# Performance work log

Measured on AMD Instinct MI355X. Metric: run time of the kernel, lower is better.

Reference implementation:

```python
import jax, jax.numpy as jnp
import numpy as np
import math

MASK_FILL = -1e6  # d2l masked_softmax fills masked scores with -1e6


def setup_inputs() -> dict:
    key = jax.random.key(0)
    kq, kk, kv, kl = jax.random.split(key, 4)
    B, Lq, Lk, D = 16, 2048, 2048, 64
    queries = jax.random.normal(kq, (B, Lq, D), dtype=jnp.float32)
    keys = jax.random.normal(kk, (B, Lk, D), dtype=jnp.float32)
    values = jax.random.normal(kv, (B, Lk, D), dtype=jnp.float32)
    valid_lens = jax.random.randint(kl, (B,), 1, Lk + 1, dtype=jnp.int32)
    return {"queries": queries, "keys": keys, "values": values, "valid_lens": valid_lens}


def reference(queries, keys, values, valid_lens):
    # scores: [B, Lq, Lk]
    d = queries.shape[-1]
    scores = jnp.einsum("bqd,bkd->bqk", queries, keys) / math.sqrt(d)
    # masked_softmax: positions >= valid_lens[b] along key axis get -1e6
    Lk = keys.shape[1]
    mask = jnp.arange(Lk)[None, None, :] < valid_lens[:, None, None]  # [B,1,Lk]
    scores = jnp.where(mask, scores, MASK_FILL)
    attn = jax.nn.softmax(scores, axis=-1)
    # dropout p=0.0 (eval) is identity
    return jnp.einsum("bqk,bkd->bqd", attn, values)
```

## Files before the change

kernel.cpp:

```cpp
#include <hip/hip_runtime.h>
#include <hip/hip_bf16.h>
#include <stdint.h>


#define BATCH 16
#define SEQ   2048
#define DIM   64
#define QBLK  32
#define NSPLIT 4
#define NTHR  256

typedef __bf16 bf16x8 __attribute__((ext_vector_type(8)));
typedef float  f32x16 __attribute__((ext_vector_type(16)));
typedef unsigned int u32x2 __attribute__((ext_vector_type(2)));

static constexpr float QSCALE = 0.125f * 1.44269504088896340736f;

__device__ __forceinline__ uint32_t pk2bf(float a, float b) {
    union { __hip_bfloat162 h; uint32_t u; } c;
    c.h = __float22bfloat162_rn(make_float2(a, b));
    return c.u;
}
__device__ __forceinline__ bf16x8 mk8(uint32_t w0, uint32_t w1, uint32_t w2, uint32_t w3) {
    union { uint32_t u[4]; bf16x8 v; } c;
    c.u[0] = w0; c.u[1] = w1; c.u[2] = w2; c.u[3] = w3;
    return c.v;
}
__device__ __forceinline__ u32x2 plswap(uint32_t a, uint32_t b) {
    return __builtin_amdgcn_permlane32_swap(a, b, false, false);
}
__device__ __forceinline__ float vmax16(const f32x16& v) {
    float a = fmaxf(fmaxf(v[0], v[1]), fmaxf(v[2], v[3]));
    float b = fmaxf(fmaxf(v[4], v[5]), fmaxf(v[6], v[7]));
    float c = fmaxf(fmaxf(v[8], v[9]), fmaxf(v[10], v[11]));
    float d = fmaxf(fmaxf(v[12], v[13]), fmaxf(v[14], v[15]));
    return fmaxf(fmaxf(a, b), fmaxf(c, d));
}
__device__ __forceinline__ float vsum16(const f32x16& v) {
    float a = (v[0] + v[1]) + (v[2] + v[3]);
    float b = (v[4] + v[5]) + (v[6] + v[7]);
    float c = (v[8] + v[9]) + (v[10] + v[11]);
    float d = (v[12] + v[13]) + (v[14] + v[15]);
    return (a + b) + (c + d);
}

__global__ __launch_bounds__(256) void prep_kv(
        const float* __restrict__ K, const float* __restrict__ V,
        unsigned short* __restrict__ Kbf, unsigned short* __restrict__ Vt)
{
    __shared__ float tl[64][65];
    const int bid = blockIdx.x;
    const int b  = bid >> 5;
    const int kb = (bid & 31) * 64;
    const int tid = threadIdx.x;

    const float* Kp = K + ((size_t)b * SEQ + kb) * DIM;
    const float* Vp = V + ((size_t)b * SEQ + kb) * DIM;
    unsigned short* Ko = Kbf + ((size_t)b * SEQ + kb) * DIM;
    unsigned short* Vo = Vt + (size_t)b * SEQ * DIM + (size_t)(kb >> 5) * 2048;

    #pragma unroll
    for (int p = 0; p < 4; ++p) {
        int idx = p * 256 + tid;
        float4 x = ((const float4*)Kp)[idx];
        ((uint2*)Ko)[idx] = make_uint2(pk2bf(x.x, x.y), pk2bf(x.z, x.w));
    }
    #pragma unroll
    for (int p = 0; p < 4; ++p) {
        int idx = p * 256 + tid;
        int r = idx >> 4, c = (idx & 15) * 4;
        float4 x = *(const float4*)(Vp + r * DIM + c);
        tl[r][c] = x.x; tl[r][c+1] = x.y; tl[r][c+2] = x.z; tl[r][c+3] = x.w;
    }
    __syncthreads();
    #pragma unroll
    for (int p = 0; p < 4; ++p) {
        int idx = p * 256 + tid;
        int sub = idx >> 9;
        int rem = idx & 511;
        int d  = rem >> 3;
        int kq = (rem & 7) * 4;
        int kr = sub * 32 + kq;
        *(uint2*)(Vo + sub * 2048 + d * 32 + kq) =
            make_uint2(pk2bf(tl[kr][d],     tl[kr + 1][d]),
                       pk2bf(tl[kr + 2][d], tl[kr + 3][d]));
    }
}

__global__ __launch_bounds__(NTHR, 2) void attn_main(
        const float* __restrict__ Q, const unsigned short* __restrict__ Kbf,
        const unsigned short* __restrict__ Vt, const int* __restrict__ VL,
        float* __restrict__ O)
{
    __shared__ float comb[NSPLIT - 1][2176];

    const int tid  = threadIdx.x;
    const int idx  = blockIdx.x;
    const int g    = idx >> 8;
    const int u    = idx & 255;
    const int b    = ((u & 15) + g) & (BATCH - 1);
    const int qt   = (u >> 4) + g * 16;
    const int qb   = qt * QBLK;
    const int split = tid >> 6;
    const int lane = tid & 63;
    const int h    = lane >> 5;
    const int ln   = lane & 31;

    const int valid  = VL[b];
    const int ntiles = (valid + 31) >> 5;

    const size_t bOff = (size_t)b * SEQ * DIM;
    const int qrow = qb + ln;

    bf16x8 qf[4];
    {
        const float* qp = Q + bOff + (size_t)qrow * DIM;
        #pragma unroll
        for (int s = 0; s < 4; ++s) {
            int c0 = s * 16 + h * 8;
            float4 x = *(const float4*)(qp + c0);
            float4 y = *(const float4*)(qp + c0 + 4);
            qf[s] = mk8(pk2bf(x.x * QSCALE, x.y * QSCALE),
                        pk2bf(x.z * QSCALE, x.w * QSCALE),
                        pk2bf(y.x * QSCALE, y.y * QSCALE),
                        pk2bf(y.z * QSCALE, y.w * QSCALE));
        }
    }

    f32x16 o0, o1;
    #pragma unroll
    for (int r = 0; r < 16; ++r) { o0[r] = 0.0f; o1[r] = 0.0f; }
    float m_run = -1e30f, l_run = 0.0f;

    const unsigned short* kp = Kbf + bOff + (size_t)ln * DIM + h * 8;
    const unsigned short* vp = Vt  + bOff + (size_t)ln * 32  + h * 8;

    bf16x8 ka[4], va[4];
    int kt = split;
    if (kt < ntiles) {
        const unsigned short* kq = kp + (size_t)kt * 2048;
        const unsigned short* vq = vp + (size_t)kt * 2048;
        #pragma unroll
        for (int s = 0; s < 4; ++s) ka[s] = *(const bf16x8*)(kq + s * 16);
        va[0] = *(const bf16x8*)(vq);
        va[1] = *(const bf16x8*)(vq + 16);
        va[2] = *(const bf16x8*)(vq + 1024);
        va[3] = *(const bf16x8*)(vq + 1024 + 16);
    }

    for (; kt < ntiles; kt += NSPLIT) {
        const int ktn = (kt + NSPLIT < ntiles) ? kt + NSPLIT : kt;
        bf16x8 kan[4], van[4];
        {
            const unsigned short* kq = kp + (size_t)ktn * 2048;
            const unsigned short* vq = vp + (size_t)ktn * 2048;
            #pragma unroll
            for (int s = 0; s < 4; ++s) kan[s] = *(const bf16x8*)(kq + s * 16);
            van[0] = *(const bf16x8*)(vq);
            van[1] = *(const bf16x8*)(vq + 16);
            van[2] = *(const bf16x8*)(vq + 1024);
            van[3] = *(const bf16x8*)(vq + 1024 + 16);
        }

        f32x16 st;
        #pragma unroll
        for (int r = 0; r < 16; ++r) st[r] = 0.0f;
        #pragma unroll
        for (int s = 0; s < 4; ++s)
            st = __builtin_amdgcn_mfma_f32_32x32x16_bf16(ka[s], qf[s], st, 0, 0, 0);

        const int kb = kt * 32;
        if (kb + 32 > valid) {
            #pragma unroll
            for (int r = 0; r < 16; ++r) {
                int krel = (r & 3) + 8 * (r >> 2) + 4 * h;
                if (kb + krel >= valid) st[r] = -1e30f;
            }
        }

        float pm = vmax16(st);
        u32x2 sm = plswap(__float_as_uint(pm), __float_as_uint(pm));
        pm = fmaxf(__uint_as_float(sm[0]), __uint_as_float(sm[1]));
        if (!__all(pm <= m_run + 8.0f)) {
            float mnew = fmaxf(m_run, pm);
            float sc = __builtin_exp2f(m_run - mnew);
            l_run *= sc;
            #pragma unroll
            for (int r = 0; r < 16; ++r) { o0[r] *= sc; o1[r] *= sc; }
            m_run = mnew;
        }
        #pragma unroll
        for (int r = 0; r < 16; ++r) st[r] = __builtin_exp2f(st[r] - m_run);
        float ps = vsum16(st);
        u32x2 ss = plswap(__float_as_uint(ps), __float_as_uint(ps));
        l_run += __uint_as_float(ss[0]) + __uint_as_float(ss[1]);

        uint32_t W00 = pk2bf(st[0],  st[1]),  W01 = pk2bf(st[2],  st[3]);
        uint32_t W10 = pk2bf(st[4],  st[5]),  W11 = pk2bf(st[6],  st[7]);
        uint32_t W20 = pk2bf(st[8],  st[9]),  W21 = pk2bf(st[10], st[11]);
        uint32_t W30 = pk2bf(st[12], st[13]), W31 = pk2bf(st[14], st[15]);
        u32x2 sA = plswap(W00, W10), sB = plswap(W01, W11);
        bf16x8 bp0 = mk8(sA[0], sB[0], sA[1], sB[1]);
        u32x2 sC = plswap(W20, W30), sD = plswap(W21, W31);
        bf16x8 bp1 = mk8(sC[0], sD[0], sC[1], sD[1]);

        o0 = __builtin_amdgcn_mfma_f32_32x32x16_bf16(va[0], bp0, o0, 0, 0, 0);
        o1 = __builtin_amdgcn_mfma_f32_32x32x16_bf16(va[2], bp0, o1, 0, 0, 0);
        o0 = __builtin_amdgcn_mfma_f32_32x32x16_bf16(va[1], bp1, o0, 0, 0, 0);
        o1 = __builtin_amdgcn_mfma_f32_32x32x16_bf16(va[3], bp1, o1, 0, 0, 0);

        #pragma unroll
        for (int i = 0; i < 4; ++i) { ka[i] = kan[i]; va[i] = van[i]; }
    }

    if (split != 0) {
        float* base = comb[split - 1];
        #pragma unroll
        for (int r = 0; r < 16; ++r) {
            base[r * 64 + lane]        = o0[r];
            base[(r + 16) * 64 + lane] = o1[r];
        }
        base[2048 + lane]      = m_run;
        base[2048 + 64 + lane] = l_run;
    }
    __syncthreads();
    if (split == 0) {
        float M = m_run;
        #pragma unroll
        for (int j = 0; j < NSPLIT - 1; ++j)
            M = fmaxf(M, comb[j][2048 + lane]);
        float sc0 = __builtin_exp2f(m_run - M);
        float lt = l_run * sc0;
        #pragma unroll
        for (int r = 0; r < 16; ++r) { o0[r] *= sc0; o1[r] *= sc0; }
        #pragma unroll
        for (int j = 0; j < NSPLIT - 1; ++j) {
            float mj = comb[j][2048 + lane];
            float lj = comb[j][2048 + 64 + lane];
            float scj = __builtin_exp2f(mj - M);
            lt += lj * scj;
            #pragma unroll
            for (int r = 0; r < 16; ++r) {
                o0[r] += scj * comb[j][r * 64 + lane];
                o1[r] += scj * comb[j][(r + 16) * 64 + lane];
            }
        }
        float inv = 1.0f / lt;
        float* op = O + bOff + (size_t)qrow * DIM;
        #pragma unroll
        for (int a = 0; a < 4; ++a) {
            float4 w0, w1;
            w0.x = o0[4*a+0] * inv; w0.y = o0[4*a+1] * inv;
            w0.z = o0[4*a+2] * inv; w0.w = o0[4*a+3] * inv;
            w1.x = o1[4*a+0] * inv; w1.y = o1[4*a+1] * inv;
            w1.z = o1[4*a+2] * inv; w1.w = o1[4*a+3] * inv;
            *(float4*)(op + 8*a + 4*h)      = w0;
            *(float4*)(op + 32 + 8*a + 4*h) = w1;
        }
    }
}

__device__ __forceinline__ uint32_t swz(uint32_t row, uint32_t colByte) {
    return row * 128u + (colByte ^ ((row & 7u) << 4));
}
__device__ __forceinline__ bf16x8 lds8(const char* p) {
    union { uint4 q; bf16x8 v; } c;
    c.q = *(const uint4*)p;
    return c.v;
}

__global__ __launch_bounds__(256, 2) void attn_fallback(
        const float* __restrict__ Q, const float* __restrict__ K,
        const float* __restrict__ V, const int* __restrict__ VL,
        float* __restrict__ O)
{
    __shared__ unsigned short lds[2][2][64 * DIM];
    const int tid  = threadIdx.x;
    const int bid  = blockIdx.x;
    const int b    = bid & (BATCH - 1);
    const int qt   = bid >> 4;
    const int qb   = qt * 64;
    const int qhalf = (tid >> 6) & 1;
    const int split = tid >> 7;
    const int lane = tid & 63;
    const int h    = lane >> 5;
    const int ln   = lane & 31;
    const int ptid = tid & 127;

    const int valid  = VL[b];
    const int ntiles = (valid + 63) / 64;
    const int nit    = (ntiles + 1) / 2;

    const size_t bOff = (size_t)b * SEQ * DIM;
    const int qrow = qb + qhalf * 32 + ln;

    bf16x8 qf[4];
    {
        const float* qp = Q + bOff + (size_t)qrow * DIM;
        #pragma unroll
        for (int s = 0; s < 4; ++s) {
            int c0 = s * 16 + h * 8;
            float4 x = *(const float4*)(qp + c0);
            float4 y = *(const float4*)(qp + c0 + 4);
            qf[s] = mk8(pk2bf(x.x * QSCALE, x.y * QSCALE),
                        pk2bf(x.z * QSCALE, x.w * QSCALE),
                        pk2bf(y.x * QSCALE, y.y * QSCALE),
                        pk2bf(y.z * QSCALE, y.w * QSCALE));
        }
    }
    f32x16 o0, o1;
    #pragma unroll
    for (int r = 0; r < 16; ++r) { o0[r] = 0.0f; o1[r] = 0.0f; }
    float m_run = -1e30f, l_run = 0.0f;
    const float* Kb = K + bOff;
    const float* Vb = V + bOff;
    char* kls = (char*)lds[split][0];
    char* vls = (char*)lds[split][1];

    for (int it = 0; it < nit; ++it) {
        const int kt = it * 2 + split;
        const bool act = kt < ntiles;
        const int kb = kt * 64;
        if (act) {
            #pragma unroll
            for (int p = 0; p < 8; ++p) {
                int idx = p * 128 + ptid;
                int r = idx >> 4, c = (idx & 15) * 4;
                float4 kx = *(const float4*)(Kb + (size_t)(kb + r) * DIM + c);
                *(uint2*)(kls + swz(r, c * 2)) =
                    make_uint2(pk2bf(kx.x, kx.y), pk2bf(kx.z, kx.w));
            }
            #pragma unroll
            for (int p = 0; p < 2; ++p) {
                int idx = p * 128 + ptid;
                int cq = idx & 15, rq = idx >> 4;
                const float* vp = Vb + (size_t)(kb + rq * 4) * DIM + cq * 4;
                float4 v0 = *(const float4*)(vp);
                float4 v1 = *(const float4*)(vp + DIM);
                float4 v2 = *(const float4*)(vp + 2 * DIM);
                float4 v3 = *(const float4*)(vp + 3 * DIM);
                float a0[4] = {v0.x, v0.y, v0.z, v0.w};
                float a1[4] = {v1.x, v1.y, v1.z, v1.w};
                float a2[4] = {v2.x, v2.y, v2.z, v2.w};
                float a3[4] = {v3.x, v3.y, v3.z, v3.w};
                #pragma unroll
                for (int i = 0; i < 4; ++i)
                    *(uint2*)(vls + swz(cq * 4 + i, rq * 8)) =
                        make_uint2(pk2bf(a0[i], a1[i]), pk2bf(a2[i], a3[i]));
            }
        }
        __syncthreads();
        if (act) {
            f32x16 st0, st1;
            #pragma unroll
            for (int r = 0; r < 16; ++r) { st0[r] = 0.0f; st1[r] = 0.0f; }
            #pragma unroll
            for (int s = 0; s < 4; ++s) {
                int cb = (s * 16 + h * 8) * 2;
                bf16x8 ka0 = lds8(kls + swz(ln,      cb));
                bf16x8 ka1 = lds8(kls + swz(ln + 32, cb));
                st0 = __builtin_amdgcn_mfma_f32_32x32x16_bf16(ka0, qf[s], st0, 0, 0, 0);
                st1 = __builtin_amdgcn_mfma_f32_32x32x16_bf16(ka1, qf[s], st1, 0, 0, 0);
            }
            if (kb + 64 > valid) {
                #pragma unroll
                for (int r = 0; r < 16; ++r) {
                    int krel = (r & 3) + 8 * (r >> 2) + 4 * h;
                    if (kb + krel      >= valid) st0[r] = -1e30f;
                    if (kb + 32 + krel >= valid) st1[r] = -1e30f;
                }
            }
            float pm = fmaxf(vmax16(st0), vmax16(st1));
            u32x2 sm = plswap(__float_as_uint(pm), __float_as_uint(pm));
            pm = fmaxf(__uint_as_float(sm[0]), __uint_as_float(sm[1]));
            float mnew = fmaxf(m_run, pm);
            float sc = __builtin_exp2f(m_run - mnew);
            #pragma unroll
            for (int r = 0; r < 16; ++r) {
                st0[r] = __builtin_exp2f(st0[r] - mnew);
                st1[r] = __builtin_exp2f(st1[r] - mnew);
            }
            float ps = vsum16(st0) + vsum16(st1);
            u32x2 ss = plswap(__float_as_uint(ps), __float_as_uint(ps));
            ps = __uint_as_float(ss[0]) + __uint_as_float(ss[1]);
            l_run = l_run * sc + ps;
            m_run = mnew;
            #pragma unroll
            for (int r = 0; r < 16; ++r) { o0[r] *= sc; o1[r] *= sc; }
            bf16x8 bp[4];
            {
                uint32_t u0 = pk2bf(st0[0], st0[1]),  u1 = pk2bf(st0[2], st0[3]);
                uint32_t u2 = pk2bf(st0[4], st0[5]),  u3 = pk2bf(st0[6], st0[7]);
                uint32_t u4 = pk2bf(st0[8], st0[9]),  u5 = pk2bf(st0[10], st0[11]);
                uint32_t u6 = pk2bf(st0[12], st0[13]), u7 = pk2bf(st0[14], st0[15]);
                u32x2 s02 = plswap(u0, u2), s13 = plswap(u1, u3);
                bp[0] = mk8(s02[0], s13[0], s02[1], s13[1]);
                u32x2 s46 = plswap(u4, u6), s57 = plswap(u5, u7);
                bp[1] = mk8(s46[0], s57[0], s46[1], s57[1]);
            }
            {
                uint32_t u0 = pk2bf(st1[0], st1[1]),  u1 = pk2bf(st1[2], st1[3]);
                uint32_t u2 = pk2bf(st1[4], st1[5]),  u3 = pk2bf(st1[6], st1[7]);
                uint32_t u4 = pk2bf(st1[8], st1[9]),  u5 = pk2bf(st1[10], st1[11]);
                uint32_t u6 = pk2bf(st1[12], st1[13]), u7 = pk2bf(st1[14], st1[15]);
                u32x2 s02 = plswap(u0, u2), s13 = plswap(u1, u3);
                bp[2] = mk8(s02[0], s13[0], s02[1], s13[1]);
                u32x2 s46 = plswap(u4, u6), s57 = plswap(u5, u7);
                bp[3] = mk8(s46[0], s57[0], s46[1], s57[1]);
            }
            #pragma unroll
            for (int x = 0; x < 4; ++x) {
                int cb = (x * 16 + h * 8) * 2;
                bf16x8 va0 = lds8(vls + swz(ln,      cb));
                bf16x8 va1 = lds8(vls + swz(ln + 32, cb));
                o0 = __builtin_amdgcn_mfma_f32_32x32x16_bf16(va0, bp[x], o0, 0, 0, 0);
                o1 = __builtin_amdgcn_mfma_f32_32x32x16_bf16(va1, bp[x], o1, 0, 0, 0);
            }
        }
        __syncthreads();
    }
    const int CSTRIDE = 32 * 64 + 128;
    float* comb = (float*)lds;
    if (split != 0) {
        float* base = comb + (size_t)qhalf * CSTRIDE;
        #pragma unroll
        for (int r = 0; r < 16; ++r) {
            base[r * 64 + lane]        = o0[r];
            base[(r + 16) * 64 + lane] = o1[r];
        }
        base[2048 + lane]      = m_run;
        base[2048 + 64 + lane] = l_run;
    }
    __syncthreads();
    if (split == 0) {
        float* base = comb + (size_t)qhalf * CSTRIDE;
        float mj = base[2048 + lane];
        float lj = base[2048 + 64 + lane];
        float M  = fmaxf(m_run, mj);
        float sc0 = __builtin_exp2f(m_run - M);
        float scj = __builtin_exp2f(mj - M);
        float lt = l_run * sc0 + lj * scj;
        float inv = 1.0f / lt;
        float* op = O + bOff + (size_t)qrow * DIM;
        #pragma unroll
        for (int a = 0; a < 4; ++a) {
            float4 w0, w1;
            w0.x = (o0[4*a+0]*sc0 + scj*base[(4*a+0)*64 + lane]) * inv;
            w0.y = (o0[4*a+1]*sc0 + scj*base[(4*a+1)*64 + lane]) * inv;
            w0.z = (o0[4*a+2]*sc0 + scj*base[(4*a+2)*64 + lane]) * inv;
            w0.w = (o0[4*a+3]*sc0 + scj*base[(4*a+3)*64 + lane]) * inv;
            w1.x = (o1[4*a+0]*sc0 + scj*base[(4*a+16)*64 + lane]) * inv;
            w1.y = (o1[4*a+1]*sc0 + scj*base[(4*a+17)*64 + lane]) * inv;
            w1.z = (o1[4*a+2]*sc0 + scj*base[(4*a+18)*64 + lane]) * inv;
            w1.w = (o1[4*a+3]*sc0 + scj*base[(4*a+19)*64 + lane]) * inv;
            *(float4*)(op + 8*a + 4*h)      = w0;
            *(float4*)(op + 32 + 8*a + 4*h) = w1;
        }
    }
}

extern "C" void kernel_launch(void* const* d_in, const int* in_sizes, int n_in,
                              void* d_out, int out_size, void* d_ws, size_t ws_size,
                              hipStream_t stream) {
    const float* q  = (const float*)d_in[0];
    const float* k  = (const float*)d_in[1];
    const float* v  = (const float*)d_in[2];
    const int*   vl = (const int*)d_in[3];
    float* out = (float*)d_out;

    const size_t KBYTES = (size_t)BATCH * SEQ * DIM * 2;
    if (ws_size >= 2 * KBYTES) {
        unsigned short* kbf = (unsigned short*)d_ws;
        unsigned short* vt  = (unsigned short*)((char*)d_ws + KBYTES);
        hipLaunchKernelGGL(prep_kv, dim3(BATCH * (SEQ / 64)), dim3(256), 0, stream,
                           k, v, kbf, vt);
        hipLaunchKernelGGL(attn_main, dim3(BATCH * (SEQ / QBLK)), dim3(NTHR), 0, stream,
                           q, kbf, vt, vl, out);
    } else {
        hipLaunchKernelGGL(attn_fallback, dim3(BATCH * (SEQ / 64)), dim3(256), 0, stream,
                           q, k, v, vl, out);
    }
}
```

Before: 49.17 us.

## Use persistent blocks with atomic work queue ordered longest-batch-first

Replaces the static one-block-per-query-tile grid with 512 persistent blocks that take work items from a global atomic counter. prep_kv now also sorts batches by valid length in descending order, so the longest items are handed out first. The goal is better load balance across CUs when valid_lens differ between batches. In exchange it adds an atomic, an extra barrier per item, and a dependence on the workspace being large enough for the counter and order array.

```diff
diff --git a/kernel.cpp b/kernel.cpp
--- a/kernel.cpp
+++ b/kernel.cpp
@@ -6,9 +6,9 @@
 #define BATCH 16
 #define SEQ   2048
 #define DIM   64
-#define QBLK  32
 #define NSPLIT 4
 #define NTHR  256
+#define NITEMS 1024
 
 typedef __bf16 bf16x8 __attribute__((ext_vector_type(8)));
 typedef float  f32x16 __attribute__((ext_vector_type(16)));
@@ -46,13 +46,31 @@
 
 __global__ __launch_bounds__(256) void prep_kv(
         const float* __restrict__ K, const float* __restrict__ V,
-        unsigned short* __restrict__ Kbf, unsigned short* __restrict__ Vt)
+        const int* __restrict__ VL,
+        unsigned short* __restrict__ Kbf, unsigned short* __restrict__ Vt,
+        unsigned int* __restrict__ counter, int* __restrict__ order)
 {
     __shared__ float tl[64][65];
     const int bid = blockIdx.x;
     const int b  = bid >> 5;
     const int kb = (bid & 31) * 64;
     const int tid = threadIdx.x;
+
+    if (bid == 0 && tid == 0) {
+        *counter = 0u;
+        int idxs[BATCH], vals[BATCH];
+        #pragma unroll
+        for (int i = 0; i < BATCH; ++i) { idxs[i] = i; vals[i] = VL[i]; }
+        for (int i = 1; i < BATCH; ++i) {
+            int vi = vals[i], xi = idxs[i], j = i - 1;
+            while (j >= 0 && vals[j] < vi) {
+                vals[j + 1] = vals[j]; idxs[j + 1] = idxs[j]; --j;
+            }
+            vals[j + 1] = vi; idxs[j + 1] = xi;
+        }
+        #pragma unroll
+        for (int i = 0; i < BATCH; ++i) order[i] = idxs[i];
+    }
 
     const float* Kp = K + ((size_t)b * SEQ + kb) * DIM;
     const float* Vp = V + ((size_t)b * SEQ + kb) * DIM;
@@ -90,173 +108,178 @@
 __global__ __launch_bounds__(NTHR, 2) void attn_main(
         const float* __restrict__ Q, const unsigned short* __restrict__ Kbf,
         const unsigned short* __restrict__ Vt, const int* __restrict__ VL,
-        float* __restrict__ O)
+        float* __restrict__ O, unsigned int* __restrict__ counter,
+        const int* __restrict__ order)
 {
     __shared__ float comb[NSPLIT - 1][2176];
+    __shared__ int item_s;
 
     const int tid  = threadIdx.x;
-    const int idx  = blockIdx.x;
-    const int g    = idx >> 8;
-    const int u    = idx & 255;
-    const int b    = ((u & 15) + g) & (BATCH - 1);
-    const int qt   = (u >> 4) + g * 16;
-    const int qb   = qt * QBLK;
     const int split = tid >> 6;
     const int lane = tid & 63;
     const int h    = lane >> 5;
     const int ln   = lane & 31;
 
-    const int valid  = VL[b];
-    const int ntiles = (valid + 31) >> 5;
-
-    const size_t bOff = (size_t)b * SEQ * DIM;
-    const int qrow = qb + ln;
-
-    bf16x8 qf[4];
-    {
-        const float* qp = Q + bOff + (size_t)qrow * DIM;
+    for (;;) {
+        if (tid == 0) item_s = (int)atomicAdd(counter, 1u);
+        __syncthreads();
+        const int item = item_s;
+        if (item >= NITEMS) break;
+
+        const int b  = order[item >> 6];
+        const int qt = item & 63;
+        const int valid  = VL[b];
+        const int ntiles = (valid + 31) >> 5;
+        const size_t bOff = (size_t)b * SEQ * DIM;
+        const int qrow = qt * 32 + ln;
+
+        bf16x8 qf[4];
+        {
+            const float* qp = Q + bOff + (size_t)qrow * DIM;
+            #pragma unroll
+            for (int s = 0; s < 4; ++s) {
+                int c0 = s * 16 + h * 8;
+                float4 x = *(const float4*)(qp + c0);
+                float4 y = *(const float4*)(qp + c0 + 4);
+                qf[s] = mk8(pk2bf(x.x * QSCALE, x.y * QSCALE),
+                            pk2bf(x.z * QSCALE, x.w * QSCALE),
+                            pk2bf(y.x * QSCALE, y.y * QSCALE),
+                            pk2bf(y.z * QSCALE, y.w * QSCALE));
+            }
+        }
+
+        f32x16 o0, o1;
         #pragma unroll
-        for (int s = 0; s < 4; ++s) {
-            int c0 = s * 16 + h * 8;
-            float4 x = *(const float4*)(qp + c0);
-            float4 y = *(const float4*)(qp + c0 + 4);
-            qf[s] = mk8(pk2bf(x.x * QSCALE, x.y * QSCALE),
-                        pk2bf(x.z * QSCALE, x.w * QSCALE),
-                        pk2bf(y.x * QSCALE, y.y * QSCALE),
-                        pk2bf(y.z * QSCALE, y.w * QSCALE));
-        }
-    }
-
-    f32x16 o0, o1;
-    #pragma unroll
-    for (int r = 0; r < 16; ++r) { o0[r] = 0.0f; o1[r] = 0.0f; }
-    float m_run = -1e30f, l_run = 0.0f;
-
-    const unsigned short* kp = Kbf + bOff + (size_t)ln * DIM + h * 8;
-    const unsigned short* vp = Vt  + bOff + (size_t)ln * 32  + h * 8;
-
-    bf16x8 ka[4], va[4];
-    int kt = split;
-    if (kt < ntiles) {
-        const unsigned short* kq = kp + (size_t)kt * 2048;
-        const unsigned short* vq = vp + (size_t)kt * 2048;
-        #pragma unroll
-        for (int s = 0; s < 4; ++s) ka[s] = *(const bf16x8*)(kq + s * 16);
-        va[0] = *(const bf16x8*)(vq);
-        va[1] = *(const bf16x8*)(vq + 16);
-        va[2] = *(const bf16x8*)(vq + 1024);
-        va[3] = *(const bf16x8*)(vq + 1024 + 16);
-    }
-
-    for (; kt < ntiles; kt += NSPLIT) {
-        const int ktn = (kt + NSPLIT < ntiles) ? kt + NSPLIT : kt;
-        bf16x8 kan[4], van[4];
-        {
-            const unsigned short* kq = kp + (size_t)ktn * 2048;
-            const unsigned short* vq = vp + (size_t)ktn * 2048;
-            #pragma unroll
-            for (int s = 0; s < 4; ++s) kan[s] = *(const bf16x8*)(kq + s * 16);
-            van[0] = *(const bf16x8*)(vq);
-            van[1] = *(const bf16x8*)(vq + 16);
-            van[2] = *(const bf16x8*)(vq + 1024);
-            van[3] = *(const bf16x8*)(vq + 1024 + 16);
-        }
-
-        f32x16 st;
-        #pragma unroll
-        for (int r = 0; r < 16; ++r) st[r] = 0.0f;
-        #pragma unroll
-        for (int s = 0; s < 4; ++s)
-            st = __builtin_amdgcn_mfma_f32_32x32x16_bf16(ka[s], qf[s], st, 0, 0, 0);
-
-        const int kb = kt * 32;
-        if (kb + 32 > valid) {
+        for (int r = 0; r < 16; ++r) { o0[r] = 0.0f; o1[r] = 0.0f; }
+        float m_run = -1e30f, l_run = 0.0f;
+
+        const unsigned short* kp = Kbf + bOff + (size_t)ln * DIM + h * 8;
+        const unsigned short* vp = Vt  + bOff + (size_t)ln * 32  + h * 8;
+
+        bf16x8 ka[4], va[4];
+        int kt = split;
+        if (kt < ntiles) {
+            const unsigned short* kq = kp + (size_t)kt * 2048;
+            const unsigned short* vq = vp + (size_t)kt * 2048;
+            #pragma unroll
+            for (int s = 0; s < 4; ++s) ka[s] = *(const bf16x8*)(kq + s * 16);
+            va[0] = *(const bf16x8*)(vq);
+            va[1] = *(const bf16x8*)(vq + 16);
+            va[2] = *(const bf16x8*)(vq + 1024);
+            va[3] = *(const bf16x8*)(vq + 1024 + 16);
+        }
+
+        for (; kt < ntiles; kt += NSPLIT) {
+            const int ktn = (kt + NSPLIT < ntiles) ? kt + NSPLIT : kt;
+            bf16x8 kan[4], van[4];
+            {
+                const unsigned short* kq = kp + (size_t)ktn * 2048;
+                const unsigned short* vq = vp + (size_t)ktn * 2048;
+                #pragma unroll
+                for (int s = 0; s < 4; ++s) kan[s] = *(const bf16x8*)(kq + s * 16);
+                van[0] = *(const bf16x8*)(vq);
+                van[1] = *(const bf16x8*)(vq + 16);
+                van[2] = *(const bf16x8*)(vq + 1024);
+                van[3] = *(const bf16x8*)(vq + 1024 + 16);
+            }
+
+            f32x16 st;
+            #pragma unroll
+            for (int r = 0; r < 16; ++r) st[r] = 0.0f;
+            #pragma unroll
+            for (int s = 0; s < 4; ++s)
+                st = __builtin_amdgcn_mfma_f32_32x32x16_bf16(ka[s], qf[s], st, 0, 0, 0);
+
+            const int kb = kt * 32;
+            if (kb + 32 > valid) {
+                #pragma unroll
+                for (int r = 0; r < 16; ++r) {
+                    int krel = (r & 3) + 8 * (r >> 2) + 4 * h;
+                    if (kb + krel >= valid) st[r] = -1e30f;
+                }
+            }
+
+            float pm = vmax16(st);
+            u32x2 sm = plswap(__float_as_uint(pm), __float_as_uint(pm));
+            pm = fmaxf(__uint_as_float(sm[0]), __uint_as_float(sm[1]));
+            if (!__all(pm <= m_run + 8.0f)) {
+                float mnew = fmaxf(m_run, pm);
+                float sc = __builtin_exp2f(m_run - mnew);
+                l_run *= sc;
+                #pragma unroll
+                for (int r = 0; r < 16; ++r) { o0[r] *= sc; o1[r] *= sc; }
+                m_run = mnew;
+            }
+            #pragma unroll
+            for (int r = 0; r < 16; ++r) st[r] = __builtin_exp2f(st[r] - m_run);
+            float ps = vsum16(st);
+            u32x2 ss = plswap(__float_as_uint(ps), __float_as_uint(ps));
+            l_run += __uint_as_float(ss[0]) + __uint_as_float(ss[1]);
+
+            uint32_t W00 = pk2bf(st[0],  st[1]),  W01 = pk2bf(st[2],  st[3]);
+            uint32_t W10 = pk2bf(st[4],  st[5]),  W11 = pk2bf(st[6],  st[7]);
+            uint32_t W20 = pk2bf(st[8],  st[9]),  W21 = pk2bf(st[10], st[11]);
+            uint32_t W30 = pk2bf(st[12], st[13]), W31 = pk2bf(st[14], st[15]);
+            u32x2 sA = plswap(W00, W10), sB = plswap(W01, W11);
+            bf16x8 bp0 = mk8(sA[0], sB[0], sA[1], sB[1]);
+            u32x2 sC = plswap(W20, W30), sD = plswap(W21, W31);
+            bf16x8 bp1 = mk8(sC[0], sD[0], sC[1], sD[1]);
+
+            o0 = __builtin_amdgcn_mfma_f32_32x32x16_bf16(va[0], bp0, o0, 0, 0, 0);
+            o1 = __builtin_amdgcn_mfma_f32_32x32x16_bf16(va[2], bp0, o1, 0, 0, 0);
+            o0 = __builtin_amdgcn_mfma_f32_32x32x16_bf16(va[1], bp1, o0, 0, 0, 0);
+            o1 = __builtin_amdgcn_mfma_f32_32x32x16_bf16(va[3], bp1, o1, 0, 0, 0);
+
+            #pragma unroll
+            for (int i = 0; i < 4; ++i) { ka[i] = kan[i]; va[i] = van[i]; }
+        }
+
+        if (split != 0) {
+            float* base = comb[split - 1];
             #pragma unroll
             for (int r = 0; r < 16; ++r) {
-                int krel = (r & 3) + 8 * (r >> 2) + 4 * h;
-                if (kb + krel >= valid) st[r] = -1e30f;
-            }
-        }
-
-        float pm = vmax16(st);
-        u32x2 sm = plswap(__float_as_uint(pm), __float_as_uint(pm));
-        pm = fmaxf(__uint_as_float(sm[0]), __uint_as_float(sm[1]));
-        if (!__all(pm <= m_run + 8.0f)) {
-            float mnew = fmaxf(m_run, pm);
-            float sc = __builtin_exp2f(m_run - mnew);
-            l_run *= sc;
-            #pragma unroll
-            for (int r = 0; r < 16; ++r) { o0[r] *= sc; o1[r] *= sc; }
-            m_run = mnew;
-        }
-        #pragma unroll
-        for (int r = 0; r < 16; ++r) st[r] = __builtin_exp2f(st[r] - m_run);
-        float ps = vsum16(st);
-        u32x2 ss = plswap(__float_as_uint(ps), __float_as_uint(ps));
-        l_run += __uint_as_float(ss[0]) + __uint_as_float(ss[1]);
-
-        uint32_t W00 = pk2bf(st[0],  st[1]),  W01 = pk2bf(st[2],  st[3]);
-        uint32_t W10 = pk2bf(st[4],  st[5]),  W11 = pk2bf(st[6],  st[7]);
-        uint32_t W20 = pk2bf(st[8],  st[9]),  W21 = pk2bf(st[10], st[11]);
-        uint32_t W30 = pk2bf(st[12], st[13]), W31 = pk2bf(st[14], st[15]);
-        u32x2 sA = plswap(W00, W10), sB = plswap(W01, W11);
-        bf16x8 bp0 = mk8(sA[0], sB[0], sA[1], sB[1]);
-        u32x2 sC = plswap(W20, W30), sD = plswap(W21, W31);
-        bf16x8 bp1 = mk8(sC[0], sD[0], sC[1], sD[1]);
-
-        o0 = __builtin_amdgcn_mfma_f32_32x32x16_bf16(va[0], bp0, o0, 0, 0, 0);
-        o1 = __builtin_amdgcn_mfma_f32_32x32x16_bf16(va[2], bp0, o1, 0, 0, 0);
-        o0 = __builtin_amdgcn_mfma_f32_32x32x16_bf16(va[1], bp1, o0, 0, 0, 0);
-        o1 = __builtin_amdgcn_mfma_f32_32x32x16_bf16(va[3], bp1, o1, 0, 0, 0);
-
-        #pragma unroll
-        for (int i = 0; i < 4; ++i) { ka[i] = kan[i]; va[i] = van[i]; }
-    }
-
-    if (split != 0) {
-        float* base = comb[split - 1];
-        #pragma unroll
-        for (int r = 0; r < 16; ++r) {
-            base[r * 64 + lane]        = o0[r];
-            base[(r + 16) * 64 + lane] = o1[r];
-        }
-        base[2048 + lane]      = m_run;
-        base[2048 + 64 + lane] = l_run;
-    }
-    __syncthreads();
-    if (split == 0) {
-        float M = m_run;
-        #pragma unroll
-        for (int j = 0; j < NSPLIT - 1; ++j)
-            M = fmaxf(M, comb[j][2048 + lane]);
-        float sc0 = __builtin_exp2f(m_run - M);
-        float lt = l_run * sc0;
-        #pragma unroll
-        for (int r = 0; r < 16; ++r) { o0[r] *= sc0; o1[r] *= sc0; }
-        #pragma unroll
-        for (int j = 0; j < NSPLIT - 1; ++j) {
-            float mj = comb[j][2048 + lane];
-            float lj = comb[j][2048 + 64 + lane];
-            float scj = __builtin_exp2f(mj - M);
-            lt += lj * scj;
-            #pragma unroll
-            for (int r = 0; r < 16; ++r) {
-                o0[r] += scj * comb[j][r * 64 + lane];
-                o1[r] += scj * comb[j][(r + 16) * 64 + lane];
-            }
-        }
-        float inv = 1.0f / lt;
-        float* op = O + bOff + (size_t)qrow * DIM;
-        #pragma unroll
-        for (int a = 0; a < 4; ++a) {
-            float4 w0, w1;
-            w0.x = o0[4*a+0] * inv; w0.y = o0[4*a+1] * inv;
-            w0.z = o0[4*a+2] * inv; w0.w = o0[4*a+3] * inv;
-            w1.x = o1[4*a+0] * inv; w1.y = o1[4*a+1] * inv;
-            w1.z = o1[4*a+2] * inv; w1.w = o1[4*a+3] * inv;
-            *(float4*)(op + 8*a + 4*h)      = w0;
-            *(float4*)(op + 32 + 8*a + 4*h) = w1;
-        }
+                base[r * 64 + lane]        = o0[r];
+                base[(r + 16) * 64 + lane] = o1[r];
+            }
+            base[2048 + lane]      = m_run;
+            base[2048 + 64 + lane] = l_run;
+        }
+        __syncthreads();
+        if (split == 0) {
+            float M = m_run;
+            #pragma unroll
+            for (int j = 0; j < NSPLIT - 1; ++j)
+                M = fmaxf(M, comb[j][2048 + lane]);
+            float sc0 = __builtin_exp2f(m_run - M);
+            float lt = l_run * sc0;
+            #pragma unroll
+            for (int r = 0; r < 16; ++r) { o0[r] *= sc0; o1[r] *= sc0; }
+            #pragma unroll
+            for (int j = 0; j < NSPLIT - 1; ++j) {
+                float mj = comb[j][2048 + lane];
+                float lj = comb[j][2048 + 64 + lane];
+                float scj = __builtin_exp2f(mj - M);
+                lt += lj * scj;
+                #pragma unroll
+                for (int r = 0; r < 16; ++r) {
+                    o0[r] += scj * comb[j][r * 64 + lane];
+                    o1[r] += scj * comb[j][(r + 16) * 64 + lane];
+                }
+            }
+            float inv = 1.0f / lt;
+            float* op = O + bOff + (size_t)qrow * DIM;
+            #pragma unroll
+            for (int a = 0; a < 4; ++a) {
+                float4 w0, w1;
+                w0.x = o0[4*a+0] * inv; w0.y = o0[4*a+1] * inv;
+                w0.z = o0[4*a+2] * inv; w0.w = o0[4*a+3] * inv;
+                w1.x = o1[4*a+0] * inv; w1.y = o1[4*a+1] * inv;
+                w1.z = o1[4*a+2] * inv; w1.w = o1[4*a+3] * inv;
+                *(float4*)(op + 8*a + 4*h)      = w0;
+                *(float4*)(op + 32 + 8*a + 4*h) = w1;
+            }
+        }
+        __syncthreads();
     }
 }
 
@@ -469,13 +492,15 @@
     float* out = (float*)d_out;
 
     const size_t KBYTES = (size_t)BATCH * SEQ * DIM * 2;
-    if (ws_size >= 2 * KBYTES) {
+    if (ws_size >= 2 * KBYTES + 256) {
         unsigned short* kbf = (unsigned short*)d_ws;
         unsigned short* vt  = (unsigned short*)((char*)d_ws + KBYTES);
+        unsigned int* counter = (unsigned int*)((char*)d_ws + 2 * KBYTES);
+        int* order = (int*)((char*)d_ws + 2 * KBYTES + 64);
         hipLaunchKernelGGL(prep_kv, dim3(BATCH * (SEQ / 64)), dim3(256), 0, stream,
-                           k, v, kbf, vt);
-        hipLaunchKernelGGL(attn_main, dim3(BATCH * (SEQ / QBLK)), dim3(NTHR), 0, stream,
-                           q, kbf, vt, vl, out);
+                           k, v, vl, kbf, vt, counter, order);
+        hipLaunchKernelGGL(attn_main, dim3(512), dim3(NTHR), 0, stream,
+                           q, kbf, vt, vl, out, counter, order);
     } else {
         hipLaunchKernelGGL(attn_fallback, dim3(BATCH * (SEQ / 64)), dim3(256), 0, stream,
                            q, k, v, vl, out);
```

Measured after the change: 59.19 us. 20.4% more time.
